# Kernel tuning notes

Hardware: AMD Instinct MI355X
Metric: run time of the kernel (lower is better)

The kernel has to match this reference:

```python
import jax, jax.numpy as jnp
import numpy as np

LOG_2PI = float(np.log(2.0 * np.pi))
EPS = 1e-6


def setup_inputs() -> dict:
    key = jax.random.key(0)
    ks = jax.random.split(key, 7)
    T, D, S = 24, 262144, 12
    recog_J = jax.random.uniform(ks[0], (T, D), minval=0.5, maxval=1.5)  # positive precisions
    recog_h = jax.random.normal(ks[1], (T, D)) * 0.1
    loc = jax.random.normal(ks[2], (D,)) * 0.1
    Tau = 1.0 + 0.1 * jax.random.normal(ks[3], (D,))
    Lambda = 1.0 + 0.1 * jax.random.normal(ks[4], (S, D))
    A = 0.9 + 0.05 * jax.random.normal(ks[5], (S, D))
    b = 0.1 * jax.random.normal(ks[6], (S, D))
    return {"recog_J": recog_J, "recog_h": recog_h, "loc": loc, "Tau": Tau,
            "Lambda": Lambda, "A": A, "b": b}


def _tile(x, T):
    # concat([x, x[:-1]]) as in the module, truncated to the T-1 transitions
    return jnp.concatenate([x, x[:-1]], axis=0)[: T - 1]


def reference(recog_J, recog_h, loc, Tau, Lambda, A, b):
    T, D = recog_J.shape
    tau = Tau ** 2 + EPS                      # init precision (D,)
    tau_mu = tau * loc
    lam = Lambda ** 2 + EPS                   # transition precision (12, D)
    # natural params of pairwise potential -lam/2 (x' - A x - b)^2 (constants dropped)
    Jaa = _tile(A ** 2 * lam, T)              # (T-1, D) precision on x_t
    Jab = _tile(A * lam, T)                   # cross term (+Jab x_t x_{t+1})
    Jbb = _tile(lam, T)                       # precision on x_{t+1}
    ha = _tile(-(A * lam * b), T)             # linear on x_t
    hb = _tile(lam * b, T)                    # linear on x_{t+1}

    # ---- forward information filter over the chain (scalar Kalman per dim) ----
    fJ0 = tau + recog_J[0]
    fh0 = tau_mu + recog_h[0]

    def fstep(carry, inp):
        fJ, fh, logZ = carry
        jaa, jab, jbb, ha_t, hb_t, rJ, rh = inp
        denom = fJ + jaa
        hc = fh + ha_t
        logZ = logZ + 0.5 * (LOG_2PI - jnp.log(denom)) + hc ** 2 / (2.0 * denom)
        fJn = jbb - jab ** 2 / denom + rJ
        fhn = hb_t + jab * hc / denom + rh
        return (fJn, fhn, logZ), (fJn, fhn)

    (fJT, fhT, logZ_acc), (fJs, fhs) = jax.lax.scan(
        fstep, (fJ0, fh0, jnp.zeros_like(fJ0)),
        (Jaa, Jab, Jbb, ha, hb, recog_J[1:], recog_h[1:]))
    fJ_all = jnp.concatenate([fJ0[None], fJs], axis=0)  # (T, D) filtered precision
    fh_all = jnp.concatenate([fh0[None], fhs], axis=0)  # (T, D) filtered h
    q_logZ = jnp.sum(logZ_acc + 0.5 * (LOG_2PI - jnp.log(fJT)) + fhT ** 2 / (2.0 * fJT))

    # ---- backward (RTS) smoother: E[x_t], E[x_t^2] ----
    ExT = fhT / fJT
    VarT = 1.0 / fJT

    def bstep(carry, inp):
        Exn, Varn = carry
        fJ, fh, jaa, jab, ha_t = inp
        denom = fJ + jaa
        g = jab / denom
        Ex = (fh + ha_t + jab * Exn) / denom
        Var = 1.0 / denom + g ** 2 * Varn
        return (Ex, Var), (Ex, Var)

    _, (Ex_rest, Var_rest) = jax.lax.scan(
        bstep, (ExT, VarT), (fJ_all[:-1], fh_all[:-1], Jaa, Jab, ha), reverse=True)
    Ex = jnp.concatenate([Ex_rest, ExT[None]], axis=0)
    Exx = jnp.concatenate([Var_rest, VarT[None]], axis=0) + Ex ** 2

    # ---- backward posterior sampling (temp = 1) ----
    eps = jax.random.normal(jax.random.key(0), (T, D), dtype=recog_J.dtype)
    zT = ExT + eps[-1] / jnp.sqrt(fJT)

    def sstep(zn, inp):
        fJ, fh, jaa, jab, ha_t, e = inp
        denom = fJ + jaa
        z = (fh + ha_t + jab * zn) / denom + e / jnp.sqrt(denom)
        return z, z

    _, z_rest = jax.lax.scan(sstep, zT,
                             (fJ_all[:-1], fh_all[:-1], Jaa, Jab, ha, eps[:-1]),
                             reverse=True)
    z = jnp.concatenate([z_rest, zT[None]], axis=0)  # (T, D)

    # ---- prior log-normalizer (constants dropped from natural potentials) ----
    init_norm = 0.5 * (LOG_2PI * D + jnp.sum(tau * loc ** 2) - jnp.sum(jnp.log(tau)))
    trans_norm = 0.5 * (LOG_2PI * D * (T - 1)
                        + jnp.sum(_tile(lam * b ** 2, T))
                        - jnp.sum(_tile(jnp.log(lam), T)))
    p_logZ = init_norm + trans_norm

    # KL(q||p) = <recog_potentials, E_q[stats]> - q_logZ + p_logZ
    kl = jnp.sum(-0.5 * recog_J * Exx + recog_h * Ex) - q_logZ + p_logZ
    return z, kl, Ex, Exx
```

## Files before the change

### kernel.cpp

```cpp
#include <hip/hip_runtime.h>
#include <stdint.h>

#define D_DIM 262144
#define T_DIM 24
#define S_DIM 12
#define BLK 256
#define NBLK (D_DIM / BLK)

static constexpr float EPSF = 1e-6f;

__device__ __forceinline__ void tf_round(unsigned& x0, unsigned& x1, int r) {
  x0 += x1;
  x1 = (x1 << r) | (x1 >> (32 - r));
  x1 ^= x0;
}

__device__ __forceinline__ void threefry00(unsigned c0, unsigned c1,
                                           unsigned& o0, unsigned& o1) {
  const unsigned ks0 = 0u, ks1 = 0u, ks2 = 0x1BD11BDAu;
  unsigned x0 = c0 + ks0, x1 = c1 + ks1;
  tf_round(x0, x1, 13); tf_round(x0, x1, 15); tf_round(x0, x1, 26); tf_round(x0, x1, 6);
  x0 += ks1; x1 += ks2 + 1u;
  tf_round(x0, x1, 17); tf_round(x0, x1, 29); tf_round(x0, x1, 16); tf_round(x0, x1, 24);
  x0 += ks2; x1 += ks0 + 2u;
  tf_round(x0, x1, 13); tf_round(x0, x1, 15); tf_round(x0, x1, 26); tf_round(x0, x1, 6);
  x0 += ks0; x1 += ks1 + 3u;
  tf_round(x0, x1, 17); tf_round(x0, x1, 29); tf_round(x0, x1, 16); tf_round(x0, x1, 24);
  x0 += ks1; x1 += ks2 + 4u;
  tf_round(x0, x1, 13); tf_round(x0, x1, 15); tf_round(x0, x1, 26); tf_round(x0, x1, 6);
  x0 += ks2; x1 += ks0 + 5u;
  o0 = x0; o1 = x1;
}

__device__ __forceinline__ float bits_to_normal(unsigned bits) {
  const float lo = -0.99999994f;
  const float hi = 1.0f;
  unsigned fb = (bits >> 9) | 0x3f800000u;
  float f = __uint_as_float(fb) - 1.0f;
  float u = f * (hi - lo) + lo;
  u = fmaxf(lo, u);
  float w = -__logf(fmaf(-u, u, 1.0f));
  float p;
  if (w < 5.0f) {
    w = w - 2.5f;
    p = 2.81022636e-08f;
    p = fmaf(p, w, 3.43273939e-07f);
    p = fmaf(p, w, -3.5233877e-06f);
    p = fmaf(p, w, -4.39150654e-06f);
    p = fmaf(p, w, 0.00021858087f);
    p = fmaf(p, w, -0.00125372503f);
    p = fmaf(p, w, -0.00417768164f);
    p = fmaf(p, w, 0.246640727f);
    p = fmaf(p, w, 1.50140941f);
  } else {
    w = sqrtf(w) - 3.0f;
    p = -0.000200214257f;
    p = fmaf(p, w, 0.000100950558f);
    p = fmaf(p, w, 0.00134934322f);
    p = fmaf(p, w, -0.00367342844f);
    p = fmaf(p, w, 0.00573950773f);
    p = fmaf(p, w, -0.0076224613f);
    p = fmaf(p, w, 0.00943887047f);
    p = fmaf(p, w, 1.00167406f);
    p = fmaf(p, w, 2.83297682f);
  }
  return 1.41421356237309515f * (p * u);
}

__global__ __launch_bounds__(256) void pgm_lds_kernel(
    const float* __restrict__ recog_J, const float* __restrict__ recog_h,
    const float* __restrict__ loc_p, const float* __restrict__ Tau_p,
    const float* __restrict__ Lambda_p, const float* __restrict__ A_p,
    const float* __restrict__ b_p,
    float* __restrict__ z_out,
    float* __restrict__ Ex_out, float* __restrict__ Exx_out,
    float* __restrict__ kl_partials) {
  __shared__ float s_rJ[T_DIM * BLK];
  __shared__ float s_rh[T_DIM * BLK];
  __shared__ float s_kl[BLK / 64];
  const int tid = threadIdx.x;
  const int d = blockIdx.x * BLK + tid;

#pragma unroll
  for (int t = 0; t < T_DIM; ++t) {
    __builtin_amdgcn_global_load_lds(
        (const __attribute__((address_space(1))) uint32_t*)(uintptr_t)(recog_J + (size_t)t * D_DIM + d),
        (__attribute__((address_space(3))) uint32_t*)(uintptr_t)(s_rJ + t * BLK + tid),
        4, 0, 0);
    __builtin_amdgcn_global_load_lds(
        (const __attribute__((address_space(1))) uint32_t*)(uintptr_t)(recog_h + (size_t)t * D_DIM + d),
        (__attribute__((address_space(3))) uint32_t*)(uintptr_t)(s_rh + t * BLK + tid),
        4, 0, 0);
  }

  float lam[S_DIM], Aa[S_DIM], hb[S_DIM];
  float kld = 0.0f;
#pragma unroll
  for (int s = 0; s < S_DIM; ++s) {
    float L = Lambda_p[s * D_DIM + d];
    float a = A_p[s * D_DIM + d];
    float bb = b_p[s * D_DIM + d];
    float l = L * L + EPSF;
    lam[s] = l;
    Aa[s] = a;
    hb[s] = l * bb;
    float wgt = (s < 11) ? 1.0f : 0.5f;
    kld += wgt * (hb[s] * bb - __logf(l));
  }
  float tau, tau_mu;
  {
    float Tv = Tau_p[d];
    float lv = loc_p[d];
    tau = Tv * Tv + EPSF;
    tau_mu = tau * lv;
    kld += 0.5f * (tau * lv * lv - __logf(tau));
  }

  __syncthreads();

  float fJ[T_DIM], fh[T_DIM];
  fJ[0] = tau + s_rJ[tid];
  fh[0] = tau_mu + s_rh[tid];
#pragma unroll
  for (int t = 0; t < T_DIM - 1; ++t) {
    const int s = (t < 12) ? t : t - 12;
    float l = lam[s], a = Aa[s];
    float jab = a * l;
    float jaa = a * jab;
    float ha = -a * hb[s];
    float denom = fJ[t] + jaa;
    float inv = __builtin_amdgcn_rcpf(denom);
    float hc = fh[t] + ha;
    kld += 0.5f * __logf(denom) - 0.5f * hc * hc * inv;
    fJ[t + 1] = l - jab * jab * inv + s_rJ[(t + 1) * BLK + tid];
    fh[t + 1] = hb[s] + jab * hc * inv + s_rh[(t + 1) * BLK + tid];
  }
  const float fJT = fJ[T_DIM - 1];
  const float fhT = fh[T_DIM - 1];
  const float invT = __builtin_amdgcn_rcpf(fJT);
  kld += 0.5f * __logf(fJT) - 0.5f * fhT * fhT * invT;

  float eps_st[S_DIM];
  float ExT = fhT * invT;
  float VarT = invT;
  float eps23;
  {
    unsigned o0, o1;
    threefry00((unsigned)(11 * D_DIM + d), (unsigned)(23 * D_DIM + d), o0, o1);
    eps_st[11] = bits_to_normal(o0);
    eps23 = bits_to_normal(o1);
  }
  float zT = ExT + eps23 * sqrtf(invT);
  float ExxT = VarT + ExT * ExT;
  kld += -0.5f * s_rJ[(T_DIM - 1) * BLK + tid] * ExxT
         + s_rh[(T_DIM - 1) * BLK + tid] * ExT;
  z_out[(T_DIM - 1) * D_DIM + d] = zT;
  Ex_out[(T_DIM - 1) * D_DIM + d] = ExT;
  Exx_out[(T_DIM - 1) * D_DIM + d] = ExxT;

  float Exn = ExT, Varn = VarT, zn = zT;
#pragma unroll
  for (int t = T_DIM - 2; t >= 0; --t) {
    const int s = (t < 12) ? t : t - 12;
    float l = lam[s], a = Aa[s];
    float jab = a * l;
    float jaa = a * jab;
    float ha = -a * hb[s];
    float denom = fJ[t] + jaa;
    float inv = __builtin_amdgcn_rcpf(denom);
    float hc = fh[t] + ha;

    float e;
    if (t >= 12) {
      unsigned o0, o1;
      threefry00((unsigned)((t - 12) * D_DIM + d), (unsigned)(t * D_DIM + d), o0, o1);
      eps_st[t - 12] = bits_to_normal(o0);
      e = bits_to_normal(o1);
    } else {
      e = eps_st[t];
    }

    float g = jab * inv;
    float Ex = (hc + jab * Exn) * inv;
    float Var = inv + g * g * Varn;
    float zt = (hc + jab * zn) * inv + e * sqrtf(inv);
    float Exx = Var + Ex * Ex;
    kld += -0.5f * s_rJ[t * BLK + tid] * Exx + s_rh[t * BLK + tid] * Ex;

    z_out[t * D_DIM + d] = zt;
    Ex_out[t * D_DIM + d] = Ex;
    Exx_out[t * D_DIM + d] = Exx;

    Exn = Ex; Varn = Var; zn = zt;
  }

#pragma unroll
  for (int off = 32; off > 0; off >>= 1)
    kld += __shfl_down(kld, off, 64);
  if ((tid & 63) == 0)
    s_kl[tid >> 6] = kld;
  __syncthreads();
  if (tid == 0)
    kl_partials[blockIdx.x] = s_kl[0] + s_kl[1] + s_kl[2] + s_kl[3];
}

__global__ __launch_bounds__(256) void kl_reduce_kernel(
    const float* __restrict__ kl_partials, float* __restrict__ kl_out) {
  __shared__ float s_kl[BLK / 64];
  float v = 0.0f;
#pragma unroll
  for (int i = 0; i < NBLK / BLK; ++i)
    v += kl_partials[i * BLK + threadIdx.x];
#pragma unroll
  for (int off = 32; off > 0; off >>= 1)
    v += __shfl_down(v, off, 64);
  if ((threadIdx.x & 63) == 0)
    s_kl[threadIdx.x >> 6] = v;
  __syncthreads();
  if (threadIdx.x == 0)
    kl_out[0] = s_kl[0] + s_kl[1] + s_kl[2] + s_kl[3];
}

extern "C" void kernel_launch(void* const* d_in, const int* in_sizes, int n_in,
                              void* d_out, int out_size, void* d_ws, size_t ws_size,
                              hipStream_t stream) {
  const float* recog_J = (const float*)d_in[0];
  const float* recog_h = (const float*)d_in[1];
  const float* loc_p   = (const float*)d_in[2];
  const float* Tau_p   = (const float*)d_in[3];
  const float* Lambda_p = (const float*)d_in[4];
  const float* A_p     = (const float*)d_in[5];
  const float* b_p     = (const float*)d_in[6];

  float* out = (float*)d_out;
  float* z_out  = out;
  float* kl_out = out + (size_t)T_DIM * D_DIM;
  float* Ex_out = kl_out + 1;
  float* Exx_out = Ex_out + (size_t)T_DIM * D_DIM;
  float* kl_partials = (float*)d_ws;

  pgm_lds_kernel<<<dim3(NBLK), dim3(BLK), 0, stream>>>(
      recog_J, recog_h, loc_p, Tau_p, Lambda_p, A_p, b_p,
      z_out, Ex_out, Exx_out, kl_partials);
  kl_reduce_kernel<<<dim3(1), dim3(BLK), 0, stream>>>(kl_partials, kl_out);
}
```

Baseline: 47.50 us.

## Double-buffer recognition loads through LDS in chunks and recover them algebraically

The single upfront async load of all 24 timesteps of recog_J/recog_h into LDS becomes a two-slot ring of 6-timestep chunks. Later chunks are issued while the forward filter runs, with explicit vmcnt/lgkmcnt waits guarding buffer reuse. The backward pass no longer rereads recog values from LDS; it recovers them from the stored fJ/fh and the transition terms. This halves LDS per block, aiming for more resident blocks and more overlap of memory with compute. The cost is extra arithmetic and possible rounding differences in the KL sum.

```diff
diff --git a/kernel.cpp b/kernel.cpp
--- a/kernel.cpp
+++ b/kernel.cpp
@@ -6,6 +6,7 @@
 #define S_DIM 12
 #define BLK 256
 #define NBLK (D_DIM / BLK)
+#define QT 6
 
 static constexpr float EPSF = 1e-6f;
 
@@ -75,23 +76,38 @@
     float* __restrict__ z_out,
     float* __restrict__ Ex_out, float* __restrict__ Exx_out,
     float* __restrict__ kl_partials) {
-  __shared__ float s_rJ[T_DIM * BLK];
-  __shared__ float s_rh[T_DIM * BLK];
+  __shared__ float s_buf[2][2][QT * BLK];
   __shared__ float s_kl[BLK / 64];
   const int tid = threadIdx.x;
   const int d = blockIdx.x * BLK + tid;
 
-#pragma unroll
-  for (int t = 0; t < T_DIM; ++t) {
-    __builtin_amdgcn_global_load_lds(
-        (const __attribute__((address_space(1))) uint32_t*)(uintptr_t)(recog_J + (size_t)t * D_DIM + d),
-        (__attribute__((address_space(3))) uint32_t*)(uintptr_t)(s_rJ + t * BLK + tid),
-        4, 0, 0);
-    __builtin_amdgcn_global_load_lds(
-        (const __attribute__((address_space(1))) uint32_t*)(uintptr_t)(recog_h + (size_t)t * D_DIM + d),
-        (__attribute__((address_space(3))) uint32_t*)(uintptr_t)(s_rh + t * BLK + tid),
-        4, 0, 0);
-  }
+#define STAGE_Q(q)                                                             \
+  {                                                                            \
+    _Pragma("unroll")                                                          \
+    for (int tr = 0; tr < QT; ++tr) {                                          \
+      const int t_ = (q) * QT + tr;                                            \
+      __builtin_amdgcn_global_load_lds(                                        \
+          (const __attribute__((address_space(1))) uint32_t*)(uintptr_t)(      \
+              recog_J + (size_t)t_ * D_DIM + d),                               \
+          (__attribute__((address_space(3))) uint32_t*)(uintptr_t)(            \
+              &s_buf[(q) & 1][0][tr * BLK + tid]), 4, 0, 0);                   \
+      __builtin_amdgcn_global_load_lds(                                        \
+          (const __attribute__((address_space(1))) uint32_t*)(uintptr_t)(      \
+              recog_h + (size_t)t_ * D_DIM + d),                               \
+          (__attribute__((address_space(3))) uint32_t*)(uintptr_t)(            \
+              &s_buf[(q) & 1][1][tr * BLK + tid]), 4, 0, 0);                   \
+    }                                                                          \
+  }
+
+#define WAIT_VM0()                                                             \
+  asm volatile("s_waitcnt vmcnt(0)" ::: "memory");                             \
+  __builtin_amdgcn_sched_barrier(0);
+#define WAIT_LGKM0()                                                           \
+  asm volatile("s_waitcnt lgkmcnt(0)" ::: "memory");                           \
+  __builtin_amdgcn_sched_barrier(0);
+
+#define RJ(t) s_buf[((t) / QT) & 1][0][((t) % QT) * BLK + tid]
+#define RH(t) s_buf[((t) / QT) & 1][1][((t) % QT) * BLK + tid]
 
   float lam[S_DIM], Aa[S_DIM], hb[S_DIM];
   float kld = 0.0f;
@@ -116,25 +132,44 @@
     kld += 0.5f * (tau * lv * lv - __logf(tau));
   }
 
-  __syncthreads();
+  STAGE_Q(0)
+  STAGE_Q(1)
+  WAIT_VM0()
 
   float fJ[T_DIM], fh[T_DIM];
-  fJ[0] = tau + s_rJ[tid];
-  fh[0] = tau_mu + s_rh[tid];
-#pragma unroll
-  for (int t = 0; t < T_DIM - 1; ++t) {
-    const int s = (t < 12) ? t : t - 12;
-    float l = lam[s], a = Aa[s];
-    float jab = a * l;
-    float jaa = a * jab;
-    float ha = -a * hb[s];
-    float denom = fJ[t] + jaa;
-    float inv = __builtin_amdgcn_rcpf(denom);
-    float hc = fh[t] + ha;
-    kld += 0.5f * __logf(denom) - 0.5f * hc * hc * inv;
-    fJ[t + 1] = l - jab * jab * inv + s_rJ[(t + 1) * BLK + tid];
-    fh[t + 1] = hb[s] + jab * hc * inv + s_rh[(t + 1) * BLK + tid];
-  }
+  fJ[0] = tau + RJ(0);
+  fh[0] = tau_mu + RH(0);
+
+#define FSTEP(t)                                                               \
+  {                                                                            \
+    const int s = ((t) < 12) ? (t) : (t) - 12;                                 \
+    float l = lam[s], a = Aa[s];                                               \
+    float jab = a * l;                                                         \
+    float jaa = a * jab;                                                       \
+    float ha = -a * hb[s];                                                     \
+    float denom = fJ[t] + jaa;                                                 \
+    float inv = __builtin_amdgcn_rcpf(denom);                                  \
+    float hc = fh[t] + ha;                                                     \
+    kld += 0.5f * __logf(denom) - 0.5f * hc * hc * inv;                        \
+    fJ[(t) + 1] = l - jab * jab * inv + RJ((t) + 1);                           \
+    fh[(t) + 1] = hb[s] + jab * hc * inv + RH((t) + 1);                        \
+  }
+
+#pragma unroll
+  for (int t = 0; t <= 4; ++t) FSTEP(t)
+  WAIT_LGKM0()
+  STAGE_Q(2)
+#pragma unroll
+  for (int t = 5; t <= 10; ++t) FSTEP(t)
+  WAIT_VM0()
+  WAIT_LGKM0()
+  STAGE_Q(3)
+#pragma unroll
+  for (int t = 11; t <= 16; ++t) FSTEP(t)
+  WAIT_VM0()
+#pragma unroll
+  for (int t = 17; t <= 22; ++t) FSTEP(t)
+
   const float fJT = fJ[T_DIM - 1];
   const float fhT = fh[T_DIM - 1];
   const float invT = __builtin_amdgcn_rcpf(fJT);
@@ -152,13 +187,11 @@
   }
   float zT = ExT + eps23 * sqrtf(invT);
   float ExxT = VarT + ExT * ExT;
-  kld += -0.5f * s_rJ[(T_DIM - 1) * BLK + tid] * ExxT
-         + s_rh[(T_DIM - 1) * BLK + tid] * ExT;
   z_out[(T_DIM - 1) * D_DIM + d] = zT;
   Ex_out[(T_DIM - 1) * D_DIM + d] = ExT;
   Exx_out[(T_DIM - 1) * D_DIM + d] = ExxT;
 
-  float Exn = ExT, Varn = VarT, zn = zT;
+  float Exn = ExT, Varn = VarT, zn = zT, Exxp = ExxT;
 #pragma unroll
   for (int t = T_DIM - 2; t >= 0; --t) {
     const int s = (t < 12) ? t : t - 12;
@@ -170,6 +203,10 @@
     float inv = __builtin_amdgcn_rcpf(denom);
     float hc = fh[t] + ha;
 
+    float rJr = fJ[t + 1] - l + jab * jab * inv;
+    float rhr = fh[t + 1] - hb[s] - jab * hc * inv;
+    kld += -0.5f * rJr * Exxp + rhr * Exn;
+
     float e;
     if (t >= 12) {
       unsigned o0, o1;
@@ -185,14 +222,14 @@
     float Var = inv + g * g * Varn;
     float zt = (hc + jab * zn) * inv + e * sqrtf(inv);
     float Exx = Var + Ex * Ex;
-    kld += -0.5f * s_rJ[t * BLK + tid] * Exx + s_rh[t * BLK + tid] * Ex;
 
     z_out[t * D_DIM + d] = zt;
     Ex_out[t * D_DIM + d] = Ex;
     Exx_out[t * D_DIM + d] = Exx;
 
-    Exn = Ex; Varn = Var; zn = zt;
-  }
+    Exn = Ex; Varn = Var; zn = zt; Exxp = Exx;
+  }
+  kld += -0.5f * (fJ[0] - tau) * Exxp + (fh[0] - tau_mu) * Exn;
 
 #pragma unroll
   for (int off = 32; off > 0; off >>= 1)
```

Result: slower. 64.42 us (+35.6%).
